# Kernel optimization log

Measured on AMD Instinct MI355X. Metric: run time of the kernel, lower is better.

The kernel has to match this reference:

```python
import jax, jax.numpy as jnp
import numpy as np

# dims (see shape_source)
B, N, P, H, M, E, HOPS = 512, 102, 12, 256, 4, 3, 2
C_CLIP = 10.0   # logit clipping constant params['C']
T = 1.0         # temperature params['T']
NEG = -1e9


def setup_inputs() -> dict:
    key = jax.random.key(0)
    ks = jax.random.split(key, 18)
    s = 0.08  # uniform init range as in _initialize_weights, use scaled normals
    inp = {
        "node_features": jax.random.normal(ks[0], (B, N, P), jnp.float32),
        "adjacency": jax.random.uniform(ks[1], (B, E, N, N), jnp.float32),  # per-edge-cat weighted adjacency
        "mask": jax.random.randint(ks[2], (B, N), 0, 2).astype(jnp.int32),  # 1 = already scheduled / forbidden
        # encoder params
        "W_emb": jax.random.normal(ks[3], (P, H), jnp.float32) * s,
        "W_rel": jax.random.normal(ks[4], (HOPS, E, H, H), jnp.float32) * s / np.sqrt(H),
        "W_self": jax.random.normal(ks[5], (HOPS, H, H), jnp.float32) * s / np.sqrt(H),
        # multi-head glimpse params (Vec / W_q / W_ref per head)
        "Vec": jax.random.normal(ks[6], (M, H, H), jnp.float32) * s,
        "W_q": jax.random.normal(ks[7], (M, 3 * H, H), jnp.float32) * s,
        "W_ref": jax.random.normal(ks[8], (M, H, H), jnp.float32) * s,
        "W_mh": jax.random.normal(ks[9], (M * H, H), jnp.float32) * s,  # multi_head_embedding
        # final pointer params
        "Vec2": jax.random.normal(ks[10], (H,), jnp.float32) * s,
        "W_q2": jax.random.normal(ks[11], (H, H), jnp.float32) * s,
        "W_ref2": jax.random.normal(ks[12], (H, H), jnp.float32) * s,
        # learned decoder seed vectors
        "dec_input": jax.random.normal(ks[13], (H,), jnp.float32) * s,
        "v_1": jax.random.normal(ks[14], (H,), jnp.float32) * s,
    }
    return inp


def reference(node_features, adjacency, mask, W_emb, W_rel, W_self, Vec, W_q,
              W_ref, W_mh, Vec2, W_q2, W_ref2, dec_input, v_1):
    # ---- encoder: linear embedding + HOPS of relational (per-edge-category) message passing ----
    h = jnp.einsum('bnp,ph->bnh', node_features, W_emb)            # [B,N,H]
    for hop in range(HOPS):
        msg = jnp.einsum('benm,bmh->benh', adjacency, h)           # gather neighbors per edge cat
        h = jax.nn.relu(jnp.einsum('benh,ehk->bnk', msg, W_rel[hop])
                        + jnp.einsum('bnh,hk->bnk', h, W_self[hop]))
    enc = h                                                         # [B,N,H]

    # ---- decoder query: cat(graph readout, learned dec_input, learned v_1) -> 3H ----
    enc_mean = enc.mean(axis=1)                                     # [B,H]
    q_cat = jnp.concatenate([enc_mean,
                             jnp.broadcast_to(dec_input, (B, H)),
                             jnp.broadcast_to(v_1, (B, H))], axis=-1)  # [B,3H]

    # ---- multi-head additive (Bahdanau) glimpse: per-head Vec/W_q/W_ref tanh scoring ----
    q = jnp.einsum('bf,mfh->bmh', q_cat, W_q)                       # [B,M,H]
    r = jnp.einsum('bnh,mhk->bmnk', enc, W_ref)                     # [B,M,N,H]
    u = jnp.einsum('bmnh,mhk->bmnk', jnp.tanh(q[:, :, None, :] + r), Vec)
    scores = u.sum(axis=-1)                                         # [B,M,N]
    scores = jnp.where(mask[:, None, :] > 0, NEG, scores)
    a = jax.nn.softmax(scores, axis=-1)
    ctx = jnp.einsum('bmn,bnh->bmh', a, enc).reshape(B, M * H)
    query2 = ctx @ W_mh                                             # [B,H]

    # ---- final pointer head (Vec2 / W_q2 / W_ref2) ----
    u2 = jnp.einsum('h,bnh->bn', Vec2,
                    jnp.tanh((query2 @ W_q2)[:, None, :] + jnp.einsum('bnh,hk->bnk', enc, W_ref2)))
    u2 = C_CLIP * jnp.tanh(u2)                                      # logit clipping
    u2 = jnp.where(mask > 0, NEG, u2)
    log_p = jax.nn.log_softmax(u2 / T, axis=-1)                     # [B,N]
    return log_p
```

## Files before the change

kernel.cpp:

```cpp
#include <hip/hip_runtime.h>
#include <hip/hip_bf16.h>

#define B 512
#define N 102
#define Pdim 12
#define H 256
#define M 4
#define E 3
#define NEG (-1e9f)
#define RT 52224

typedef __hip_bfloat16 bf16;
typedef __attribute__((ext_vector_type(8))) short short8;
typedef __attribute__((ext_vector_type(4))) float f32x4;
typedef __attribute__((ext_vector_type(16))) float f32x16;

__device__ __forceinline__ float b2f(bf16 v) { return __bfloat162float(v); }
__device__ __forceinline__ bf16 f2b(float v) { return __float2bfloat16(v); }
__device__ __forceinline__ short f2bs(float v) {
    bf16 t = __float2bfloat16(v);
    return *reinterpret_cast<short*>(&t);
}
__device__ __forceinline__ float fast_tanh(float x) {
    float e = __expf(2.f * x);
    return 1.f - 2.f * __builtin_amdgcn_rcpf(e + 1.f);
}

__global__ __launch_bounds__(256) void wt_prep(const float* __restrict__ Wrel,
                                               const float* __restrict__ Wself,
                                               const float* __restrict__ Wref,
                                               const float* __restrict__ Wref2,
                                               const float* __restrict__ Wmh,
                                               const float* __restrict__ Wq2,
                                               short* __restrict__ wfrag,
                                               short* __restrict__ wrefT,
                                               short* __restrict__ wref2T,
                                               short* __restrict__ wmh_bf,
                                               short* __restrict__ wq2_bf) {
    int idx = blockIdx.x * 256 + threadIdx.x;
    if (idx < 524288) {
        int j = idx & 7;
        int lq = (idx >> 3) & 63;
        int ks = (idx >> 9) & 31;
        int ct = (idx >> 14) & 15;
        int hop = idx >> 18;
        int c = ct * 16 + (lq & 15);
        int k = ks * 32 + ((lq >> 4) & 3) * 8 + j;
        float v;
        if (k < 768) {
            int e = k >> 8, kk = k & 255;
            v = Wrel[(((size_t)hop * E + e) * H + kk) * H + c];
        } else {
            v = Wself[((size_t)hop * H + (k - 768)) * H + c];
        }
        wfrag[idx] = f2bs(v);
    } else if (idx < 786432) {
        int r = idx - 524288;
        int row = r >> 8, k = r & 255;
        int m = row >> 8, c = row & 255;
        wrefT[r] = f2bs(Wref[((size_t)m * H + k) * H + c]);
    } else if (idx < 851968) {
        int r = idx - 786432;
        int c = r >> 8, k = r & 255;
        wref2T[r] = f2bs(Wref2[k * H + c]);
    } else if (idx < 1114112) {
        int r = idx - 851968;
        wmh_bf[r] = f2bs(Wmh[r]);
    } else if (idx < 1179648) {
        int r = idx - 1114112;
        wq2_bf[r] = f2bs(Wq2[r]);
    }
}

__global__ __launch_bounds__(256) void embed_k(const float* __restrict__ nf,
                                               const float* __restrict__ W_emb,
                                               bf16* __restrict__ h) {
    int row = blockIdx.x;
    int k = threadIdx.x;
    __shared__ float f[Pdim];
    if (k < Pdim) f[k] = nf[(size_t)row * Pdim + k];
    __syncthreads();
    float s = 0.f;
#pragma unroll
    for (int p = 0; p < Pdim; ++p) s += f[p] * W_emb[p * H + k];
    h[(size_t)row * H + k] = f2b(s);
}

#define HP 264
#define YP 136
__global__ __launch_bounds__(512) void hop_fused(const bf16* __restrict__ hin,
                                                 const float* __restrict__ adj,
                                                 const short* __restrict__ wfragp,
                                                 bf16* __restrict__ hout) {
    int b = blockIdx.x;
    int tid = threadIdx.x;
    int w = tid >> 6;
    int l = tid & 63;
    int cg = l & 15;
    int rg = (l >> 4) & 3;

    __shared__ short hS[112 * HP];
    __shared__ short YtS[256 * YP];
    __shared__ short AsS[112 * YP];

    const short8 z8 = {0, 0, 0, 0, 0, 0, 0, 0};
    for (int i = tid; i < (112 * YP) / 8; i += 512) ((short8*)AsS)[i] = z8;
    for (int i = tid; i < 10 * 32; i += 512) {
        int n = 102 + (i >> 5), g = i & 31;
        *(short8*)(&hS[n * HP + g * 8]) = z8;
    }
    for (int i = tid; i < 512; i += 512) {
        int c = i >> 1, part = i & 1;
        *(short8*)(&YtS[c * YP + 112 + part * 8]) = z8;
    }
    const short* hp = (const short*)hin;
    for (int i = tid; i < 102 * 32; i += 512) {
        int n = i >> 5, g = i & 31;
        *(short8*)(&hS[n * HP + g * 8]) = *(const short8*)(hp + ((size_t)b * N + n) * H + g * 8);
    }
    __syncthreads();

    const short8* wf8 = (const short8*)wfragp;
    int ct0 = 2 * w, ct1 = 2 * w + 1;

    f32x4 hacc[2][7];
#pragma unroll
    for (int i = 0; i < 2; ++i)
#pragma unroll
        for (int j = 0; j < 7; ++j) hacc[i][j] = (f32x4){0.f, 0.f, 0.f, 0.f};

    for (int e = 0; e < E; ++e) {
        const float* Ab = adj + (((size_t)b * E + e) * N) * N;
        for (int i = tid; i < N * N; i += 512) {
            int n = i / N, m = i - n * N;
            AsS[n * YP + m] = f2bs(Ab[i]);
        }
        f32x4 g[2][7];
#pragma unroll
        for (int i = 0; i < 2; ++i)
#pragma unroll
            for (int j = 0; j < 7; ++j) g[i][j] = (f32x4){0.f, 0.f, 0.f, 0.f};
#pragma unroll
        for (int ks = 0; ks < 8; ++ks) {
            short8 wfa = wf8[(ct0 * 32 + e * 8 + ks) * 64 + l];
            short8 wfb = wf8[(ct1 * 32 + e * 8 + ks) * 64 + l];
#pragma unroll
            for (int mt = 0; mt < 7; ++mt) {
                short8 hf = *(const short8*)(&hS[(mt * 16 + cg) * HP + ks * 32 + rg * 8]);
                g[0][mt] = __builtin_amdgcn_mfma_f32_16x16x32_bf16(wfa, hf, g[0][mt], 0, 0, 0);
                g[1][mt] = __builtin_amdgcn_mfma_f32_16x16x32_bf16(wfb, hf, g[1][mt], 0, 0, 0);
            }
        }
#pragma unroll
        for (int ctl = 0; ctl < 2; ++ctl)
#pragma unroll
            for (int mt = 0; mt < 7; ++mt)
#pragma unroll
                for (int r = 0; r < 4; ++r) {
                    int c = (2 * w + ctl) * 16 + rg * 4 + r;
                    YtS[c * YP + mt * 16 + cg] = f2bs(g[ctl][mt][r]);
                }
        __syncthreads();
#pragma unroll
        for (int ks = 0; ks < 4; ++ks) {
            short8 yf0 = *(const short8*)(&YtS[(ct0 * 16 + cg) * YP + ks * 32 + rg * 8]);
            short8 yf1 = *(const short8*)(&YtS[(ct1 * 16 + cg) * YP + ks * 32 + rg * 8]);
#pragma unroll
            for (int nt = 0; nt < 7; ++nt) {
                short8 af = *(const short8*)(&AsS[(nt * 16 + cg) * YP + ks * 32 + rg * 8]);
                hacc[0][nt] = __builtin_amdgcn_mfma_f32_16x16x32_bf16(af, yf0, hacc[0][nt], 0, 0, 0);
                hacc[1][nt] = __builtin_amdgcn_mfma_f32_16x16x32_bf16(af, yf1, hacc[1][nt], 0, 0, 0);
            }
        }
        __syncthreads();
    }
#pragma unroll
    for (int ks = 0; ks < 8; ++ks) {
        short8 wfa = wf8[(ct0 * 32 + 24 + ks) * 64 + l];
        short8 wfb = wf8[(ct1 * 32 + 24 + ks) * 64 + l];
#pragma unroll
        for (int nt = 0; nt < 7; ++nt) {
            short8 hf = *(const short8*)(&hS[(nt * 16 + cg) * HP + ks * 32 + rg * 8]);
            hacc[0][nt] = __builtin_amdgcn_mfma_f32_16x16x32_bf16(hf, wfa, hacc[0][nt], 0, 0, 0);
            hacc[1][nt] = __builtin_amdgcn_mfma_f32_16x16x32_bf16(hf, wfb, hacc[1][nt], 0, 0, 0);
        }
    }
    __syncthreads();
#pragma unroll
    for (int ctl = 0; ctl < 2; ++ctl)
#pragma unroll
        for (int nt = 0; nt < 7; ++nt)
#pragma unroll
            for (int r = 0; r < 4; ++r) {
                int n = nt * 16 + rg * 4 + r;
                int c = w * 32 + ctl * 16 + cg;
                float v = hacc[ctl][nt][r];
                hS[n * HP + c] = f2bs(v > 0.f ? v : 0.f);
            }
    __syncthreads();
    short* ho = (short*)hout;
    for (int i = tid; i < 102 * 32; i += 512) {
        int n = i >> 5, g = i & 31;
        *(short8*)(ho + ((size_t)b * N + n) * H + g * 8) = *(const short8*)(&hS[n * HP + g * 8]);
    }
}

__global__ __launch_bounds__(256, 2) void head2_mfma(const bf16* __restrict__ X,
                                                     const short* __restrict__ WT,
                                                     const float* __restrict__ qb, int qbs,
                                                     const float* __restrict__ vsb,
                                                     float* __restrict__ outp, int obs) {
    int rt = blockIdx.x, m = blockIdx.y;
    int r0 = rt * 128;
    int tid = threadIdx.x;
    int w = tid >> 6, l = tid & 63;
    int lr = l & 31;
    int lh = l >> 5;
    __shared__ short Xs[128 * 256];
    __shared__ float qls[3 * 256];
    __shared__ float part[4][128];

    const short* Xp = (const short*)X;
#pragma unroll
    for (int i = 0; i < 16; ++i) {
        int id = tid + i * 256;
        int r = id >> 5, g = id & 31;
        short8 v = *(const short8*)(Xp + (size_t)(r0 + r) * H + g * 8);
        *(short8*)((char*)Xs + r * 512 + ((g ^ (r & 7)) * 16)) = v;
    }
    int b_base = r0 / N;
#pragma unroll
    for (int i = 0; i < 3; ++i) {
        int bb = b_base + i;
        if (bb > B - 1) bb = B - 1;
        qls[i * 256 + tid] = qb[(size_t)bb * qbs + m * H + tid];
    }
    const short8* w8 = (const short8*)WT;
    int cbase = m * 256 + w * 64;
    short8 afr0[16], afr1[16];
#pragma unroll
    for (int ks = 0; ks < 16; ++ks) {
        afr0[ks] = w8[(size_t)(cbase + lr) * 32 + ks * 2 + lh];
        afr1[ks] = w8[(size_t)(cbase + 32 + lr) * 32 + ks * 2 + lh];
    }
    float vsl[32];
#pragma unroll
    for (int j = 0; j < 16; ++j) {
        int cl = (j & 3) + 8 * (j >> 2) + 4 * lh;
        vsl[j]      = vsb[m * H + w * 64 + cl];
        vsl[16 + j] = vsb[m * H + w * 64 + 32 + cl];
    }
    __syncthreads();

    int swz = lr & 7;
    for (int t = 0; t < 4; ++t) {
        f32x16 acc0, acc1;
#pragma unroll
        for (int j = 0; j < 16; ++j) { acc0[j] = 0.f; acc1[j] = 0.f; }
        const char* xbase = (const char*)Xs + (t * 32 + lr) * 512;
#pragma unroll
        for (int ks = 0; ks < 16; ++ks) {
            short8 bx = *(const short8*)(xbase + (((2 * ks + lh) ^ swz) * 16));
            acc0 = __builtin_amdgcn_mfma_f32_32x32x16_bf16(afr0[ks], bx, acc0, 0, 0, 0);
            acc1 = __builtin_amdgcn_mfma_f32_32x32x16_bf16(afr1[ks], bx, acc1, 0, 0, 0);
        }
        int r = r0 + t * 32 + lr;
        int b = r / N;
        int boff = b - b_base;
        float s = 0.f;
#pragma unroll
        for (int j = 0; j < 16; ++j) {
            int cl = (j & 3) + 8 * (j >> 2) + 4 * lh;
            float x0 = qls[boff * 256 + w * 64 + cl] + acc0[j];
            s += fast_tanh(x0) * vsl[j];
            float x1 = qls[boff * 256 + w * 64 + 32 + cl] + acc1[j];
            s += fast_tanh(x1) * vsl[16 + j];
        }
        s += __shfl_xor(s, 32, 64);
        if (l < 32) part[w][t * 32 + lr] = s;
    }
    __syncthreads();
    if (tid < 128) {
        int r = r0 + tid;
        int b = r / N, n = r - b * N;
        outp[(size_t)b * obs + m * N + n] = part[0][tid] + part[1][tid] + part[2][tid] + part[3][tid];
    }
}

__global__ __launch_bounds__(256) void mean_k(const bf16* __restrict__ enc,
                                              float* __restrict__ enc_mean) {
    int b = blockIdx.x, k = threadIdx.x;
    float s = 0.f;
    for (int n = 0; n < N; ++n) s += b2f(enc[((size_t)b * N + n) * H + k]);
    enc_mean[(size_t)b * H + k] = s * (1.f / (float)N);
}

__global__ __launch_bounds__(256) void prep_k(const float* __restrict__ W_q,
                                              const float* __restrict__ Vec,
                                              const float* __restrict__ dec,
                                              const float* __restrict__ v1,
                                              float* __restrict__ qconst,
                                              float* __restrict__ vsum) {
    int m = blockIdx.x, hh = threadIdx.x;
    __shared__ float dls[H], vls[H];
    dls[hh] = dec[hh];
    vls[hh] = v1[hh];
    __syncthreads();
    const float* Wm = W_q + (size_t)m * (3 * H) * H;
    float s = 0.f;
    for (int f = 0; f < H; ++f)
        s += dls[f] * Wm[(H + f) * H + hh] + vls[f] * Wm[(2 * H + f) * H + hh];
    qconst[m * H + hh] = s;
    float vs = 0.f;
    const float* Vr = Vec + ((size_t)m * H + hh) * H;
    for (int k = 0; k < H; ++k) vs += Vr[k];
    vsum[m * H + hh] = vs;
}

__global__ __launch_bounds__(256) void q_k(const float* __restrict__ enc_mean,
                                           const float* __restrict__ W_q,
                                           const float* __restrict__ qconst,
                                           float* __restrict__ qbuf) {
    int bid = blockIdx.x;
    int b = bid >> 2, m = bid & 3;
    int hh = threadIdx.x;
    __shared__ float em[H];
    em[hh] = enc_mean[(size_t)b * H + hh];
    __syncthreads();
    const float* Wm = W_q + (size_t)m * (3 * H) * H;
    float s = qconst[m * H + hh];
    for (int f = 0; f < H; ++f) s += em[f] * Wm[f * H + hh];
    qbuf[((size_t)b * M + m) * H + hh] = s;
}

__global__ __launch_bounds__(256) void softmax_ctx_k(const float* __restrict__ scores,
                                                     const int* __restrict__ mask,
                                                     const bf16* __restrict__ enc,
                                                     float* __restrict__ ctx) {
    int bid = blockIdx.x;
    int b = bid >> 2, m = bid & 3;
    int tid = threadIdx.x;
    __shared__ float a[128];
    __shared__ float red[2];
    float sv = NEG;
    if (tid < N)
        sv = (mask[(size_t)b * N + tid] > 0) ? NEG : scores[((size_t)b * M + m) * N + tid];
    if (tid < 128) a[tid] = sv;
    __syncthreads();
    if (tid < 64) {
        float v = fmaxf(a[tid], a[tid + 64]);
        v = fmaxf(v, __shfl_xor(v, 32, 64));
        v = fmaxf(v, __shfl_xor(v, 16, 64));
        v = fmaxf(v, __shfl_xor(v, 8, 64));
        v = fmaxf(v, __shfl_xor(v, 4, 64));
        v = fmaxf(v, __shfl_xor(v, 2, 64));
        v = fmaxf(v, __shfl_xor(v, 1, 64));
        if (tid == 0) red[0] = v;
    }
    __syncthreads();
    float mx = red[0];
    float ev = (tid < N) ? __expf(sv - mx) : 0.f;
    if (tid < 128) a[tid] = ev;
    __syncthreads();
    if (tid < 64) {
        float v = a[tid] + a[tid + 64];
        v += __shfl_xor(v, 32, 64);
        v += __shfl_xor(v, 16, 64);
        v += __shfl_xor(v, 8, 64);
        v += __shfl_xor(v, 4, 64);
        v += __shfl_xor(v, 2, 64);
        v += __shfl_xor(v, 1, 64);
        if (tid == 0) red[1] = __builtin_amdgcn_rcpf(v);
    }
    __syncthreads();
    float inv = red[1];
    float c = 0.f;
    for (int n = 0; n < N; ++n)
        c += a[n] * b2f(enc[((size_t)b * N + n) * H + tid]);
    ctx[((size_t)b * M + m) * H + tid] = c * inv;
}

__global__ __launch_bounds__(256) void query2_k(const float* __restrict__ ctx,
                                                const short* __restrict__ wmh,
                                                const short* __restrict__ wq2,
                                                float* __restrict__ q2) {
    int b = blockIdx.x;
    int tid = threadIdx.x;
    __shared__ float cx[M * H];
    __shared__ float qy[H];
    for (int idx = tid; idx < M * H; idx += 256) cx[idx] = ctx[(size_t)b * M * H + idx];
    __syncthreads();
    const bf16* wm = (const bf16*)wmh;
    float acc = 0.f;
    for (int j = 0; j < M * H; ++j) acc += cx[j] * b2f(wm[(size_t)j * H + tid]);
    qy[tid] = acc;
    __syncthreads();
    const bf16* w2 = (const bf16*)wq2;
    float acc2 = 0.f;
    for (int k = 0; k < H; ++k) acc2 += qy[k] * b2f(w2[(size_t)k * H + tid]);
    q2[(size_t)b * H + tid] = acc2;
}

__global__ __launch_bounds__(128) void final_out_k(const float* __restrict__ u2,
                                                   const int* __restrict__ mask,
                                                   float* __restrict__ out) {
    int b = blockIdx.x;
    int tid = threadIdx.x;
    __shared__ float sv[N];
    __shared__ float mx_s, lse_s;
    if (tid < N) {
        float u = 10.f * tanhf(u2[(size_t)b * N + tid]);
        if (mask[(size_t)b * N + tid] > 0) u = NEG;
        sv[tid] = u;
    }
    __syncthreads();
    if (tid == 0) {
        float mx = -3e38f;
        for (int n = 0; n < N; ++n) mx = fmaxf(mx, sv[n]);
        float s = 0.f;
        for (int n = 0; n < N; ++n) s += __expf(sv[n] - mx);
        mx_s = mx;
        lse_s = logf(s);
    }
    __syncthreads();
    if (tid < N) out[(size_t)b * N + tid] = (sv[tid] - mx_s) - lse_s;
}

extern "C" void kernel_launch(void* const* d_in, const int* in_sizes, int n_in,
                              void* d_out, int out_size, void* d_ws, size_t ws_size,
                              hipStream_t stream) {
    const float* nf     = (const float*)d_in[0];
    const float* adj    = (const float*)d_in[1];
    const int*   mask   = (const int*)d_in[2];
    const float* W_emb  = (const float*)d_in[3];
    const float* W_rel  = (const float*)d_in[4];
    const float* W_self = (const float*)d_in[5];
    const float* Vec    = (const float*)d_in[6];
    const float* W_q    = (const float*)d_in[7];
    const float* W_ref  = (const float*)d_in[8];
    const float* W_mh   = (const float*)d_in[9];
    const float* Vec2   = (const float*)d_in[10];
    const float* W_q2   = (const float*)d_in[11];
    const float* W_ref2 = (const float*)d_in[12];
    const float* dec    = (const float*)d_in[13];
    const float* v_1    = (const float*)d_in[14];
    float* out = (float*)d_out;

    char* p = (char*)d_ws;
    size_t off = 0;
    auto alloc = [&](size_t bytes) -> char* {
        char* q = p + off;
        off += (bytes + 255) & ~(size_t)255;
        return q;
    };
    bf16* hA    = (bf16*)alloc((size_t)RT * H * sizeof(bf16));
    bf16* hB    = (bf16*)alloc((size_t)RT * H * sizeof(bf16));
    short* wfrag  = (short*)alloc(524288 * sizeof(short));
    short* wrefT  = (short*)alloc(262144 * sizeof(short));
    short* wref2T = (short*)alloc(65536 * sizeof(short));
    short* wmh_bf = (short*)alloc(262144 * sizeof(short));
    short* wq2_bf = (short*)alloc(65536 * sizeof(short));
    float* enc_mean = (float*)alloc((size_t)B * H * sizeof(float));
    float* qconst   = (float*)alloc((size_t)M * H * sizeof(float));
    float* vsumb    = (float*)alloc((size_t)M * H * sizeof(float));
    float* qbuf     = (float*)alloc((size_t)B * M * H * sizeof(float));
    float* scoresb  = (float*)alloc((size_t)B * M * N * sizeof(float));
    float* ctxb     = (float*)alloc((size_t)B * M * H * sizeof(float));
    float* q2b      = (float*)alloc((size_t)B * H * sizeof(float));
    float* u2b      = (float*)alloc((size_t)B * N * sizeof(float));

    wt_prep<<<4608, 256, 0, stream>>>(W_rel, W_self, W_ref, W_ref2, W_mh, W_q2,
                                      wfrag, wrefT, wref2T, wmh_bf, wq2_bf);
    embed_k<<<RT, 256, 0, stream>>>(nf, W_emb, hA);

    hop_fused<<<B, 512, 0, stream>>>(hA, adj, wfrag, hB);
    hop_fused<<<B, 512, 0, stream>>>(hB, adj, wfrag + 262144, hA);

    const bf16* enc = hA;

    mean_k<<<B, 256, 0, stream>>>(enc, enc_mean);
    prep_k<<<M, 256, 0, stream>>>(W_q, Vec, dec, v_1, qconst, vsumb);
    q_k<<<B * M, 256, 0, stream>>>(enc_mean, W_q, qconst, qbuf);
    head2_mfma<<<dim3(RT / 128, M), 256, 0, stream>>>(enc, wrefT, qbuf, M * H, vsumb, scoresb, M * N);
    softmax_ctx_k<<<B * M, 256, 0, stream>>>(scoresb, mask, enc, ctxb);
    query2_k<<<B, 256, 0, stream>>>(ctxb, wmh_bf, wq2_bf, q2b);
    head2_mfma<<<dim3(RT / 128, 1), 256, 0, stream>>>(enc, wref2T, q2b, H, Vec2, u2b, N);
    final_out_k<<<B, 128, 0, stream>>>(u2b, mask, out);
}
```

Measured before the change: 317.6 us.

## Widen hop kernel, prefetch adjacency, fuse mean and prep kernels, tidy small kernels

The hop kernel moves to 1024 threads with one column tile per wave, and prefetches each adjacency slice into registers during the MFMA phase so the global loads overlap compute. The mean reduction is fused into the second hop, prep_k is folded into wt_prep, and W_q gets a bf16 copy for q_k. embed_k handles 64 rows per block with the weights held in registers, and the final log-softmax uses parallel wave reductions instead of a single thread. The larger block raises register pressure under launch_bounds(1024,4) and may reduce the number of resident blocks per CU.

```diff
diff --git a/kernel.cpp b/kernel.cpp
--- a/kernel.cpp
+++ b/kernel.cpp
@@ -9,6 +9,7 @@
 #define E 3
 #define NEG (-1e9f)
 #define RT 52224
+#define NN (N * N)
 
 typedef __hip_bfloat16 bf16;
 typedef __attribute__((ext_vector_type(8))) short short8;
@@ -32,11 +33,35 @@
                                                const float* __restrict__ Wref2,
                                                const float* __restrict__ Wmh,
                                                const float* __restrict__ Wq2,
+                                               const float* __restrict__ W_q,
+                                               const float* __restrict__ Vec,
+                                               const float* __restrict__ dec,
+                                               const float* __restrict__ v1,
                                                short* __restrict__ wfrag,
                                                short* __restrict__ wrefT,
                                                short* __restrict__ wref2T,
                                                short* __restrict__ wmh_bf,
-                                               short* __restrict__ wq2_bf) {
+                                               short* __restrict__ wq2_bf,
+                                               short* __restrict__ wq_bf,
+                                               float* __restrict__ qconst,
+                                               float* __restrict__ vsum) {
+    if (blockIdx.x >= 5632) {
+        int m = blockIdx.x - 5632, hh = threadIdx.x;
+        __shared__ float dls[H], vls[H];
+        dls[hh] = dec[hh];
+        vls[hh] = v1[hh];
+        __syncthreads();
+        const float* Wm = W_q + (size_t)m * (3 * H) * H;
+        float s = 0.f;
+        for (int f = 0; f < H; ++f)
+            s += dls[f] * Wm[(H + f) * H + hh] + vls[f] * Wm[(2 * H + f) * H + hh];
+        qconst[m * H + hh] = s;
+        float vs = 0.f;
+        const float* Vr = Vec + ((size_t)m * H + hh) * H;
+        for (int k = 0; k < H; ++k) vs += Vr[k];
+        vsum[m * H + hh] = vs;
+        return;
+    }
     int idx = blockIdx.x * 256 + threadIdx.x;
     if (idx < 524288) {
         int j = idx & 7;
@@ -69,29 +94,41 @@
     } else if (idx < 1179648) {
         int r = idx - 1114112;
         wq2_bf[r] = f2bs(Wq2[r]);
+    } else if (idx < 1441792) {
+        int r = idx - 1179648;
+        int m = r >> 16, fh = r & 65535;
+        wq_bf[r] = f2bs(W_q[(size_t)m * 768 * 256 + fh]);
     }
 }
 
 __global__ __launch_bounds__(256) void embed_k(const float* __restrict__ nf,
                                                const float* __restrict__ W_emb,
                                                bf16* __restrict__ h) {
-    int row = blockIdx.x;
-    int k = threadIdx.x;
-    __shared__ float f[Pdim];
-    if (k < Pdim) f[k] = nf[(size_t)row * Pdim + k];
-    __syncthreads();
-    float s = 0.f;
-#pragma unroll
-    for (int p = 0; p < Pdim; ++p) s += f[p] * W_emb[p * H + k];
-    h[(size_t)row * H + k] = f2b(s);
+    int r0 = blockIdx.x * 64;
+    int tid = threadIdx.x;
+    __shared__ float fs[64][Pdim];
+    for (int i = tid; i < 64 * Pdim; i += 256)
+        fs[i / Pdim][i % Pdim] = nf[(size_t)r0 * Pdim + i];
+    float w[Pdim];
+#pragma unroll
+    for (int p = 0; p < Pdim; ++p) w[p] = W_emb[p * H + tid];
+    __syncthreads();
+    for (int r = 0; r < 64; ++r) {
+        float s = 0.f;
+#pragma unroll
+        for (int p = 0; p < Pdim; ++p) s += fs[r][p] * w[p];
+        h[(size_t)(r0 + r) * H + tid] = f2b(s);
+    }
 }
 
 #define HP 264
 #define YP 136
-__global__ __launch_bounds__(512) void hop_fused(const bf16* __restrict__ hin,
-                                                 const float* __restrict__ adj,
-                                                 const short* __restrict__ wfragp,
-                                                 bf16* __restrict__ hout) {
+#define AREG 11
+__global__ __launch_bounds__(1024, 4) void hop_fused(const bf16* __restrict__ hin,
+                                                     const float* __restrict__ adj,
+                                                     const short* __restrict__ wfragp,
+                                                     bf16* __restrict__ hout,
+                                                     float* __restrict__ mean_out) {
     int b = blockIdx.x;
     int tid = threadIdx.x;
     int w = tid >> 6;
@@ -104,104 +141,123 @@
     __shared__ short AsS[112 * YP];
 
     const short8 z8 = {0, 0, 0, 0, 0, 0, 0, 0};
-    for (int i = tid; i < (112 * YP) / 8; i += 512) ((short8*)AsS)[i] = z8;
-    for (int i = tid; i < 10 * 32; i += 512) {
+    for (int i = tid; i < (112 * YP) / 8; i += 1024) ((short8*)AsS)[i] = z8;
+    for (int i = tid; i < 10 * 32; i += 1024) {
         int n = 102 + (i >> 5), g = i & 31;
         *(short8*)(&hS[n * HP + g * 8]) = z8;
     }
-    for (int i = tid; i < 512; i += 512) {
+    for (int i = tid; i < 512; i += 1024) {
         int c = i >> 1, part = i & 1;
         *(short8*)(&YtS[c * YP + 112 + part * 8]) = z8;
     }
     const short* hp = (const short*)hin;
-    for (int i = tid; i < 102 * 32; i += 512) {
+    for (int i = tid; i < 102 * 32; i += 1024) {
         int n = i >> 5, g = i & 31;
         *(short8*)(&hS[n * HP + g * 8]) = *(const short8*)(hp + ((size_t)b * N + n) * H + g * 8);
     }
+
+    int offA[AREG];
+    bool valA[AREG];
+#pragma unroll
+    for (int i = 0; i < AREG; ++i) {
+        int id = tid + (i << 10);
+        valA[i] = (id < NN);
+        int n = id / N, m = id - n * N;
+        offA[i] = valA[i] ? (n * YP + m) : 0;
+    }
+    const float* Ab0 = adj + ((size_t)b * E) * NN;
+    float areg[AREG];
+#pragma unroll
+    for (int i = 0; i < AREG; ++i) {
+        int id = tid + (i << 10);
+        areg[i] = valA[i] ? Ab0[id] : 0.f;
+    }
     __syncthreads();
 
     const short8* wf8 = (const short8*)wfragp;
-    int ct0 = 2 * w, ct1 = 2 * w + 1;
-
-    f32x4 hacc[2][7];
-#pragma unroll
-    for (int i = 0; i < 2; ++i)
-#pragma unroll
-        for (int j = 0; j < 7; ++j) hacc[i][j] = (f32x4){0.f, 0.f, 0.f, 0.f};
+
+    f32x4 hacc[7];
+#pragma unroll
+    for (int j = 0; j < 7; ++j) hacc[j] = (f32x4){0.f, 0.f, 0.f, 0.f};
 
     for (int e = 0; e < E; ++e) {
-        const float* Ab = adj + (((size_t)b * E + e) * N) * N;
-        for (int i = tid; i < N * N; i += 512) {
-            int n = i / N, m = i - n * N;
-            AsS[n * YP + m] = f2bs(Ab[i]);
-        }
-        f32x4 g[2][7];
-#pragma unroll
-        for (int i = 0; i < 2; ++i)
-#pragma unroll
-            for (int j = 0; j < 7; ++j) g[i][j] = (f32x4){0.f, 0.f, 0.f, 0.f};
+        f32x4 g[7];
+#pragma unroll
+        for (int j = 0; j < 7; ++j) g[j] = (f32x4){0.f, 0.f, 0.f, 0.f};
 #pragma unroll
         for (int ks = 0; ks < 8; ++ks) {
-            short8 wfa = wf8[(ct0 * 32 + e * 8 + ks) * 64 + l];
-            short8 wfb = wf8[(ct1 * 32 + e * 8 + ks) * 64 + l];
+            short8 wfa = wf8[(w * 32 + e * 8 + ks) * 64 + l];
 #pragma unroll
             for (int mt = 0; mt < 7; ++mt) {
                 short8 hf = *(const short8*)(&hS[(mt * 16 + cg) * HP + ks * 32 + rg * 8]);
-                g[0][mt] = __builtin_amdgcn_mfma_f32_16x16x32_bf16(wfa, hf, g[0][mt], 0, 0, 0);
-                g[1][mt] = __builtin_amdgcn_mfma_f32_16x16x32_bf16(wfb, hf, g[1][mt], 0, 0, 0);
+                g[mt] = __builtin_amdgcn_mfma_f32_16x16x32_bf16(wfa, hf, g[mt], 0, 0, 0);
             }
         }
 #pragma unroll
-        for (int ctl = 0; ctl < 2; ++ctl)
-#pragma unroll
-            for (int mt = 0; mt < 7; ++mt)
-#pragma unroll
-                for (int r = 0; r < 4; ++r) {
-                    int c = (2 * w + ctl) * 16 + rg * 4 + r;
-                    YtS[c * YP + mt * 16 + cg] = f2bs(g[ctl][mt][r]);
-                }
+        for (int i = 0; i < AREG; ++i)
+            if (valA[i]) AsS[offA[i]] = f2bs(areg[i]);
+        if (e < E - 1) {
+            const float* Abn = adj + ((size_t)b * E + e + 1) * NN;
+#pragma unroll
+            for (int i = 0; i < AREG; ++i) {
+                int id = tid + (i << 10);
+                if (valA[i]) areg[i] = Abn[id];
+            }
+        }
+#pragma unroll
+        for (int mt = 0; mt < 7; ++mt)
+#pragma unroll
+            for (int r = 0; r < 4; ++r) {
+                int c = w * 16 + rg * 4 + r;
+                YtS[c * YP + mt * 16 + cg] = f2bs(g[mt][r]);
+            }
         __syncthreads();
 #pragma unroll
         for (int ks = 0; ks < 4; ++ks) {
-            short8 yf0 = *(const short8*)(&YtS[(ct0 * 16 + cg) * YP + ks * 32 + rg * 8]);
-            short8 yf1 = *(const short8*)(&YtS[(ct1 * 16 + cg) * YP + ks * 32 + rg * 8]);
+            short8 yf = *(const short8*)(&YtS[(w * 16 + cg) * YP + ks * 32 + rg * 8]);
 #pragma unroll
             for (int nt = 0; nt < 7; ++nt) {
                 short8 af = *(const short8*)(&AsS[(nt * 16 + cg) * YP + ks * 32 + rg * 8]);
-                hacc[0][nt] = __builtin_amdgcn_mfma_f32_16x16x32_bf16(af, yf0, hacc[0][nt], 0, 0, 0);
-                hacc[1][nt] = __builtin_amdgcn_mfma_f32_16x16x32_bf16(af, yf1, hacc[1][nt], 0, 0, 0);
+                hacc[nt] = __builtin_amdgcn_mfma_f32_16x16x32_bf16(af, yf, hacc[nt], 0, 0, 0);
             }
         }
         __syncthreads();
     }
 #pragma unroll
     for (int ks = 0; ks < 8; ++ks) {
-        short8 wfa = wf8[(ct0 * 32 + 24 + ks) * 64 + l];
-        short8 wfb = wf8[(ct1 * 32 + 24 + ks) * 64 + l];
+        short8 wfa = wf8[(w * 32 + 24 + ks) * 64 + l];
 #pragma unroll
         for (int nt = 0; nt < 7; ++nt) {
             short8 hf = *(const short8*)(&hS[(nt * 16 + cg) * HP + ks * 32 + rg * 8]);
-            hacc[0][nt] = __builtin_amdgcn_mfma_f32_16x16x32_bf16(hf, wfa, hacc[0][nt], 0, 0, 0);
-            hacc[1][nt] = __builtin_amdgcn_mfma_f32_16x16x32_bf16(hf, wfb, hacc[1][nt], 0, 0, 0);
-        }
-    }
-    __syncthreads();
-#pragma unroll
-    for (int ctl = 0; ctl < 2; ++ctl)
-#pragma unroll
-        for (int nt = 0; nt < 7; ++nt)
-#pragma unroll
-            for (int r = 0; r < 4; ++r) {
-                int n = nt * 16 + rg * 4 + r;
-                int c = w * 32 + ctl * 16 + cg;
-                float v = hacc[ctl][nt][r];
-                hS[n * HP + c] = f2bs(v > 0.f ? v : 0.f);
-            }
+            hacc[nt] = __builtin_amdgcn_mfma_f32_16x16x32_bf16(hf, wfa, hacc[nt], 0, 0, 0);
+        }
+    }
+    __syncthreads();
+#pragma unroll
+    for (int nt = 0; nt < 7; ++nt)
+#pragma unroll
+        for (int r = 0; r < 4; ++r) {
+            int n = nt * 16 + rg * 4 + r;
+            int c = w * 16 + cg;
+            float v = hacc[nt][r];
+            hS[n * HP + c] = f2bs(v > 0.f ? v : 0.f);
+        }
     __syncthreads();
     short* ho = (short*)hout;
-    for (int i = tid; i < 102 * 32; i += 512) {
+    for (int i = tid; i < 102 * 32; i += 1024) {
         int n = i >> 5, g = i & 31;
         *(short8*)(ho + ((size_t)b * N + n) * H + g * 8) = *(const short8*)(&hS[n * HP + g * 8]);
+    }
+    if (mean_out) {
+        float* partf = (float*)AsS;
+        int c = tid & 255, qq = tid >> 8;
+        float s = 0.f;
+        for (int n = qq; n < N; n += 4) s += b2f(*(const bf16*)&hS[n * HP + c]);
+        partf[qq * 256 + c] = s;
+        __syncthreads();
+        if (tid < 256)
+            mean_out[(size_t)b * H + tid] =
+                (partf[tid] + partf[256 + tid] + partf[512 + tid] + partf[768 + tid]) * (1.f / (float)N);
     }
 }
 
@@ -287,38 +343,8 @@
     }
 }
 
-__global__ __launch_bounds__(256) void mean_k(const bf16* __restrict__ enc,
-                                              float* __restrict__ enc_mean) {
-    int b = blockIdx.x, k = threadIdx.x;
-    float s = 0.f;
-    for (int n = 0; n < N; ++n) s += b2f(enc[((size_t)b * N + n) * H + k]);
-    enc_mean[(size_t)b * H + k] = s * (1.f / (float)N);
-}
-
-__global__ __launch_bounds__(256) void prep_k(const float* __restrict__ W_q,
-                                              const float* __restrict__ Vec,
-                                              const float* __restrict__ dec,
-                                              const float* __restrict__ v1,
-                                              float* __restrict__ qconst,
-                                              float* __restrict__ vsum) {
-    int m = blockIdx.x, hh = threadIdx.x;
-    __shared__ float dls[H], vls[H];
-    dls[hh] = dec[hh];
-    vls[hh] = v1[hh];
-    __syncthreads();
-    const float* Wm = W_q + (size_t)m * (3 * H) * H;
-    float s = 0.f;
-    for (int f = 0; f < H; ++f)
-        s += dls[f] * Wm[(H + f) * H + hh] + vls[f] * Wm[(2 * H + f) * H + hh];
-    qconst[m * H + hh] = s;
-    float vs = 0.f;
-    const float* Vr = Vec + ((size_t)m * H + hh) * H;
-    for (int k = 0; k < H; ++k) vs += Vr[k];
-    vsum[m * H + hh] = vs;
-}
-
 __global__ __launch_bounds__(256) void q_k(const float* __restrict__ enc_mean,
-                                           const float* __restrict__ W_q,
+                                           const short* __restrict__ wq_bf,
                                            const float* __restrict__ qconst,
                                            float* __restrict__ qbuf) {
     int bid = blockIdx.x;
@@ -327,9 +353,9 @@
     __shared__ float em[H];
     em[hh] = enc_mean[(size_t)b * H + hh];
     __syncthreads();
-    const float* Wm = W_q + (size_t)m * (3 * H) * H;
+    const bf16* Wm = (const bf16*)(wq_bf + (size_t)m * 65536);
     float s = qconst[m * H + hh];
-    for (int f = 0; f < H; ++f) s += em[f] * Wm[f * H + hh];
+    for (int f = 0; f < H; ++f) s += em[f] * b2f(Wm[f * H + hh]);
     qbuf[((size_t)b * M + m) * H + hh] = s;
 }
 
@@ -406,24 +432,42 @@
                                                    float* __restrict__ out) {
     int b = blockIdx.x;
     int tid = threadIdx.x;
-    __shared__ float sv[N];
-    __shared__ float mx_s, lse_s;
+    __shared__ float a[128];
+    __shared__ float red[2];
+    float u = NEG;
     if (tid < N) {
-        float u = 10.f * tanhf(u2[(size_t)b * N + tid]);
+        u = 10.f * fast_tanh(u2[(size_t)b * N + tid]);
         if (mask[(size_t)b * N + tid] > 0) u = NEG;
-        sv[tid] = u;
-    }
-    __syncthreads();
-    if (tid == 0) {
-        float mx = -3e38f;
-        for (int n = 0; n < N; ++n) mx = fmaxf(mx, sv[n]);
-        float s = 0.f;
-        for (int n = 0; n < N; ++n) s += __expf(sv[n] - mx);
-        mx_s = mx;
-        lse_s = logf(s);
-    }
-    __syncthreads();
-    if (tid < N) out[(size_t)b * N + tid] = (sv[tid] - mx_s) - lse_s;
+    }
+    a[tid] = u;
+    __syncthreads();
+    if (tid < 64) {
+        float v = fmaxf(a[tid], a[tid + 64]);
+        v = fmaxf(v, __shfl_xor(v, 32, 64));
+        v = fmaxf(v, __shfl_xor(v, 16, 64));
+        v = fmaxf(v, __shfl_xor(v, 8, 64));
+        v = fmaxf(v, __shfl_xor(v, 4, 64));
+        v = fmaxf(v, __shfl_xor(v, 2, 64));
+        v = fmaxf(v, __shfl_xor(v, 1, 64));
+        if (tid == 0) red[0] = v;
+    }
+    __syncthreads();
+    float mx = red[0];
+    float ev = (tid < N) ? __expf(u - mx) : 0.f;
+    a[tid] = ev;
+    __syncthreads();
+    if (tid < 64) {
+        float v = a[tid] + a[tid + 64];
+        v += __shfl_xor(v, 32, 64);
+        v += __shfl_xor(v, 16, 64);
+        v += __shfl_xor(v, 8, 64);
+        v += __shfl_xor(v, 4, 64);
+        v += __shfl_xor(v, 2, 64);
+        v += __shfl_xor(v, 1, 64);
+        if (tid == 0) red[1] = logf(v);
+    }
+    __syncthreads();
+    if (tid < N) out[(size_t)b * N + tid] = (u - mx) - red[1];
 }
 
 extern "C" void kernel_launch(void* const* d_in, const int* in_sizes, int n_in,
@@ -460,6 +504,7 @@
     short* wref2T = (short*)alloc(65536 * sizeof(short));
     short* wmh_bf = (short*)alloc(262144 * sizeof(short));
     short* wq2_bf = (short*)alloc(65536 * sizeof(short));
+    short* wq_bf  = (short*)alloc(262144 * sizeof(short));
     float* enc_mean = (float*)alloc((size_t)B * H * sizeof(float));
     float* qconst   = (float*)alloc((size_t)M * H * sizeof(float));
     float* vsumb    = (float*)alloc((size_t)M * H * sizeof(float));
@@ -469,18 +514,18 @@
     float* q2b      = (float*)alloc((size_t)B * H * sizeof(float));
     float* u2b      = (float*)alloc((size_t)B * N * sizeof(float));
 
-    wt_prep<<<4608, 256, 0, stream>>>(W_rel, W_self, W_ref, W_ref2, W_mh, W_q2,
-                                      wfrag, wrefT, wref2T, wmh_bf, wq2_bf);
-    embed_k<<<RT, 256, 0, stream>>>(nf, W_emb, hA);
-
-    hop_fused<<<B, 512, 0, stream>>>(hA, adj, wfrag, hB);
-    hop_fused<<<B, 512, 0, stream>>>(hB, adj, wfrag + 262144, hA);
+    wt_prep<<<5636, 256, 0, stream>>>(W_rel, W_self, W_ref, W_ref2, W_mh, W_q2,
+                                      W_q, Vec, dec, v_1,
+                                      wfrag, wrefT, wref2T, wmh_bf, wq2_bf, wq_bf,
+                                      qconst, vsumb);
+    embed_k<<<RT / 64, 256, 0, stream>>>(nf, W_emb, hA);
+
+    hop_fused<<<B, 1024, 0, stream>>>(hA, adj, wfrag, hB, nullptr);
+    hop_fused<<<B, 1024, 0, stream>>>(hB, adj, wfrag + 262144, hA, enc_mean);
 
     const bf16* enc = hA;
 
-    mean_k<<<B, 256, 0, stream>>>(enc, enc_mean);
-    prep_k<<<M, 256, 0, stream>>>(W_q, Vec, dec, v_1, qconst, vsumb);
-    q_k<<<B * M, 256, 0, stream>>>(enc_mean, W_q, qconst, qbuf);
+    q_k<<<B * M, 256, 0, stream>>>(enc_mean, wq_bf, qconst, qbuf);
     head2_mfma<<<dim3(RT / 128, M), 256, 0, stream>>>(enc, wrefT, qbuf, M * H, vsumb, scoresb, M * N);
     softmax_ctx_k<<<B * M, 256, 0, stream>>>(scoresb, mask, enc, ctxb);
     query2_k<<<B, 256, 0, stream>>>(ctxb, wmh_bf, wq2_bf, q2b);
```

New measurement: 293.5 us. 7.6% less time.
